# Performance work log

Measured on AMD Instinct MI355X. Metric: run time of the kernel, lower is better.

Reference implementation:

```python
import jax, jax.numpy as jnp
import numpy as np

TEMPERATURE = 0.1
POS_WEIGHT = 0.3
EPS = 1e-8  # torch F.cosine_similarity eps


def setup_inputs() -> dict:
    key = jax.random.key(0)
    k1, k2, k3 = jax.random.split(key, 3)
    B, P, N, D = 256, 4, 1024, 512
    anchor = jax.random.normal(k1, (B, D), dtype=jnp.float32)
    positives = jax.random.normal(k2, (B, P, D), dtype=jnp.float32)
    negatives = jax.random.normal(k3, (B, N, D), dtype=jnp.float32)
    return {"anchor": anchor, "positives": positives, "negatives": negatives}


def _cosine_sim(a, b):
    # a: (B, 1, D), b: (B, N, D) -> (B, N)
    num = jnp.sum(a * b, axis=-1)
    den = jnp.maximum(jnp.linalg.norm(a, axis=-1) * jnp.linalg.norm(b, axis=-1), EPS)
    return num / den


def reference(anchor, positives, negatives):
    num_pos = positives.shape[1]
    a = anchor[:, None, :]                      # (B, 1, D)
    pos_sim = _cosine_sim(a, positives)         # (B, P)
    neg_sim = _cosine_sim(a, negatives)         # (B, N)
    all_sim = jnp.concatenate([pos_sim, neg_sim], axis=1)   # (B, P+N)
    probs = jax.nn.softmax(all_sim / TEMPERATURE, axis=1)   # (B, P+N)

    # rank (0-based) of each column in descending-prob order: argsort-of-argsort
    order = jnp.argsort(-probs, axis=1)         # (B, P+N) indices sorted descending
    ranks = jnp.argsort(order, axis=1)          # rank of each original column

    rr = 1.0 / (ranks[:, :num_pos].astype(jnp.float32) + 1.0)   # (B, P)
    expected_rr = jnp.sum(probs[:, :num_pos] * rr, axis=1)      # (B,)

    loss = -jnp.mean(expected_rr)
    loss = loss + POS_WEIGHT * (1.0 - jnp.mean(pos_sim))
    return loss
```

## Files before the change

kernel.cpp:

```cpp
#include <hip/hip_runtime.h>
#include <math.h>

#define B_DIM 256
#define P_DIM 4
#define N_DIM 1024
#define D_DIM 512
#define NV (P_DIM + N_DIM)
#define INV_TEMP 10.0f
#define POS_W 0.3f
#define EPS_C 1e-8f

__device__ __forceinline__ float wave_sum_f(float v) {
#pragma unroll
  for (int m = 1; m < 64; m <<= 1) v += __shfl_xor(v, m, 64);
  return v;
}

__device__ __forceinline__ float wave_max_f(float v) {
#pragma unroll
  for (int m = 1; m < 64; m <<= 1) v = fmaxf(v, __shfl_xor(v, m, 64));
  return v;
}

__device__ __forceinline__ int wave_sum_i(int v) {
#pragma unroll
  for (int m = 1; m < 64; m <<= 1) v += __shfl_xor(v, m, 64);
  return v;
}

__device__ __forceinline__ float dot4(float4 a, float4 b) {
  return a.x * b.x + a.y * b.y + a.z * b.z + a.w * b.w;
}

__global__ __launch_bounds__(1024) void rr_row_kernel(
    const float* __restrict__ anchor, const float* __restrict__ positives,
    const float* __restrict__ negatives, float* __restrict__ partials) {
  const int b = blockIdx.x;
  const int lane = threadIdx.x & 63;
  const int wave = threadIdx.x >> 6;

  __shared__ float sims[NV];

  const float4* arow = (const float4*)(anchor + (size_t)b * D_DIM);
  const float4 a0 = arow[lane];
  const float4 a1 = arow[lane + 64];
  float asq = dot4(a0, a0) + dot4(a1, a1);
  asq = wave_sum_f(asq);
  const float anorm = sqrtf(asq);

  const float* posrow = positives + (size_t)b * P_DIM * D_DIM;
  const float* negrow = negatives + (size_t)b * N_DIM * D_DIM;

#pragma unroll 1
  for (int it = 0; it < 8; ++it) {
    const int v0 = it * 128 + wave * 8;
    float4 bv[8][2];
#pragma unroll
    for (int i = 0; i < 8; ++i) {
      const int v = v0 + i;
      const float* src = (v < P_DIM) ? (posrow + (size_t)v * D_DIM)
                                     : (negrow + (size_t)(v - P_DIM) * D_DIM);
      const float4* p = (const float4*)src;
      bv[i][0] = p[lane];
      bv[i][1] = p[lane + 64];
    }
    float d[8], bq[8];
#pragma unroll
    for (int i = 0; i < 8; ++i) {
      d[i]  = dot4(a0, bv[i][0]) + dot4(a1, bv[i][1]);
      bq[i] = dot4(bv[i][0], bv[i][0]) + dot4(bv[i][1], bv[i][1]);
    }
#pragma unroll
    for (int i = 0; i < 8; ++i) {
      d[i]  = wave_sum_f(d[i]);
      bq[i] = wave_sum_f(bq[i]);
    }
    if (lane == 0) {
#pragma unroll
      for (int i = 0; i < 8; ++i) {
        const float den = fmaxf(anorm * sqrtf(bq[i]), EPS_C);
        sims[v0 + i] = d[i] / den;
      }
    }
  }

  if (wave == 0) {
#pragma unroll
    for (int i = 0; i < 4; ++i) {
      const int v = 1024 + i;
      const float4* p = (const float4*)(negrow + (size_t)(v - P_DIM) * D_DIM);
      const float4 b0 = p[lane];
      const float4 b1 = p[lane + 64];
      float d  = dot4(a0, b0) + dot4(a1, b1);
      float bq = dot4(b0, b0) + dot4(b1, b1);
      d  = wave_sum_f(d);
      bq = wave_sum_f(bq);
      if (lane == 0) {
        const float den = fmaxf(anorm * sqrtf(bq), EPS_C);
        sims[v] = d / den;
      }
    }
  }
  __syncthreads();

  if (wave == 0) {
    float m = -3.4e38f;
    for (int v = lane; v < NV; v += 64) m = fmaxf(m, sims[v] * INV_TEMP);
    m = wave_max_f(m);
    float Z = 0.0f;
    for (int v = lane; v < NV; v += 64) Z += expf(sims[v] * INV_TEMP - m);
    Z = wave_sum_f(Z);
    const float sp0 = sims[0], sp1 = sims[1], sp2 = sims[2], sp3 = sims[3];
    int c0 = 0, c1 = 0, c2 = 0, c3 = 0;
    for (int v = lane; v < NV; v += 64) {
      const float s = sims[v];
      c0 += (s > sp0);
      c1 += (s > sp1) || (s == sp1 && v < 1);
      c2 += (s > sp2) || (s == sp2 && v < 2);
      c3 += (s > sp3) || (s == sp3 && v < 3);
    }
    c0 = wave_sum_i(c0);
    c1 = wave_sum_i(c1);
    c2 = wave_sum_i(c2);
    c3 = wave_sum_i(c3);
    if (lane == 0) {
      const float invZ = 1.0f / Z;
      const float p0 = expf(sp0 * INV_TEMP - m) * invZ;
      const float p1 = expf(sp1 * INV_TEMP - m) * invZ;
      const float p2 = expf(sp2 * INV_TEMP - m) * invZ;
      const float p3 = expf(sp3 * INV_TEMP - m) * invZ;
      const float err = p0 / (float)(c0 + 1) + p1 / (float)(c1 + 1) +
                        p2 / (float)(c2 + 1) + p3 / (float)(c3 + 1);
      partials[b] = err;
      partials[B_DIM + b] = sp0 + sp1 + sp2 + sp3;
    }
  }
}

__global__ __launch_bounds__(256) void rr_finalize_kernel(
    const float* __restrict__ partials, float* __restrict__ out) {
  const int t = threadIdx.x;
  const int lane = t & 63;
  const int wave = t >> 6;
  float rr = partials[t];
  float ps = partials[B_DIM + t];
  rr = wave_sum_f(rr);
  ps = wave_sum_f(ps);
  __shared__ float srr[4], sps[4];
  if (lane == 0) { srr[wave] = rr; sps[wave] = ps; }
  __syncthreads();
  if (t == 0) {
    const float SRR = srr[0] + srr[1] + srr[2] + srr[3];
    const float SPS = sps[0] + sps[1] + sps[2] + sps[3];
    const float loss =
        -(SRR / (float)B_DIM) +
        POS_W * (1.0f - SPS / (float)(B_DIM * P_DIM));
    out[0] = loss;
  }
}

extern "C" void kernel_launch(void* const* d_in, const int* in_sizes, int n_in,
                              void* d_out, int out_size, void* d_ws, size_t ws_size,
                              hipStream_t stream) {
  const float* anchor = (const float*)d_in[0];
  const float* positives = (const float*)d_in[1];
  const float* negatives = (const float*)d_in[2];
  float* partials = (float*)d_ws;
  float* out = (float*)d_out;

  rr_row_kernel<<<B_DIM, 1024, 0, stream>>>(anchor, positives, negatives, partials);
  rr_finalize_kernel<<<1, 256, 0, stream>>>(partials, out);
}
```

Before: 677.4 us.

## Split similarity computation across many small blocks and add separate rank kernel

The per-row 1024-thread kernel is replaced by a 2D grid of 256-thread blocks, where each wave computes 4 cosine similarities and writes them to a global workspace. A new one-wave-per-row kernel then loads the similarities into registers and computes the softmax and rank counts. The goal is higher occupancy and better latency hiding for the memory-bound 537MB negatives read. The cost is an extra kernel launch, a global round trip for the similarity matrix, and fewer loads in flight per wave.

Result: no change. 677.6 us (+0.0%).

```diff
diff --git a/kernel.cpp b/kernel.cpp
--- a/kernel.cpp
+++ b/kernel.cpp
@@ -9,6 +9,8 @@
 #define INV_TEMP 10.0f
 #define POS_W 0.3f
 #define EPS_C 1e-8f
+#define VPW 4
+#define VBLK 65
 
 __device__ __forceinline__ float wave_sum_f(float v) {
 #pragma unroll
@@ -32,108 +34,112 @@
   return a.x * b.x + a.y * b.y + a.z * b.z + a.w * b.w;
 }
 
-__global__ __launch_bounds__(1024) void rr_row_kernel(
+__global__ __launch_bounds__(256, 8) void sims_kernel(
     const float* __restrict__ anchor, const float* __restrict__ positives,
-    const float* __restrict__ negatives, float* __restrict__ partials) {
-  const int b = blockIdx.x;
+    const float* __restrict__ negatives, float* __restrict__ simsg) {
+  const int b = blockIdx.y;
   const int lane = threadIdx.x & 63;
   const int wave = threadIdx.x >> 6;
-
-  __shared__ float sims[NV];
+  const int v0 = blockIdx.x * (4 * VPW) + wave * VPW;
+  if (v0 >= NV) return;
 
   const float4* arow = (const float4*)(anchor + (size_t)b * D_DIM);
   const float4 a0 = arow[lane];
   const float4 a1 = arow[lane + 64];
+
+  const float* posrow = positives + (size_t)b * P_DIM * D_DIM;
+  const float* negrow = negatives + (size_t)b * N_DIM * D_DIM;
+
   float asq = dot4(a0, a0) + dot4(a1, a1);
   asq = wave_sum_f(asq);
   const float anorm = sqrtf(asq);
 
-  const float* posrow = positives + (size_t)b * P_DIM * D_DIM;
-  const float* negrow = negatives + (size_t)b * N_DIM * D_DIM;
-
-#pragma unroll 1
-  for (int it = 0; it < 8; ++it) {
-    const int v0 = it * 128 + wave * 8;
-    float4 bv[8][2];
+  float out[VPW];
 #pragma unroll
-    for (int i = 0; i < 8; ++i) {
-      const int v = v0 + i;
-      const float* src = (v < P_DIM) ? (posrow + (size_t)v * D_DIM)
-                                     : (negrow + (size_t)(v - P_DIM) * D_DIM);
-      const float4* p = (const float4*)src;
-      bv[i][0] = p[lane];
-      bv[i][1] = p[lane + 64];
-    }
-    float d[8], bq[8];
-#pragma unroll
-    for (int i = 0; i < 8; ++i) {
-      d[i]  = dot4(a0, bv[i][0]) + dot4(a1, bv[i][1]);
-      bq[i] = dot4(bv[i][0], bv[i][0]) + dot4(bv[i][1], bv[i][1]);
-    }
-#pragma unroll
-    for (int i = 0; i < 8; ++i) {
-      d[i]  = wave_sum_f(d[i]);
-      bq[i] = wave_sum_f(bq[i]);
-    }
-    if (lane == 0) {
-#pragma unroll
-      for (int i = 0; i < 8; ++i) {
-        const float den = fmaxf(anorm * sqrtf(bq[i]), EPS_C);
-        sims[v0 + i] = d[i] / den;
-      }
-    }
+  for (int pr = 0; pr < VPW / 2; ++pr) {
+    const int va = v0 + 2 * pr;
+    const int vb = va + 1;
+    const float4* pa = (const float4*)((va < P_DIM)
+                           ? posrow + (size_t)va * D_DIM
+                           : negrow + (size_t)(va - P_DIM) * D_DIM);
+    const float4* pb = (const float4*)((vb < P_DIM)
+                           ? posrow + (size_t)vb * D_DIM
+                           : negrow + (size_t)(vb - P_DIM) * D_DIM);
+    const float4 x0 = pa[lane];
+    const float4 x1 = pa[lane + 64];
+    float da = dot4(a0, x0) + dot4(a1, x1);
+    float qa = dot4(x0, x0) + dot4(x1, x1);
+    const float4 y0 = pb[lane];
+    const float4 y1 = pb[lane + 64];
+    da = wave_sum_f(da);
+    qa = wave_sum_f(qa);
+    float db = dot4(a0, y0) + dot4(a1, y1);
+    float qb = dot4(y0, y0) + dot4(y1, y1);
+    db = wave_sum_f(db);
+    qb = wave_sum_f(qb);
+    out[2 * pr]     = da / fmaxf(anorm * sqrtf(qa), EPS_C);
+    out[2 * pr + 1] = db / fmaxf(anorm * sqrtf(qb), EPS_C);
   }
 
-  if (wave == 0) {
+  if (lane == 0) {
+    *(float4*)(simsg + (size_t)b * NV + v0) =
+        make_float4(out[0], out[1], out[2], out[3]);
+  }
+}
+
+__global__ __launch_bounds__(64) void rank_kernel(
+    const float* __restrict__ simsg, float* __restrict__ partials) {
+  const int b = blockIdx.x;
+  const int lane = threadIdx.x;
+  const float* row = simsg + (size_t)b * NV;
+
+  float s[17];
 #pragma unroll
-    for (int i = 0; i < 4; ++i) {
-      const int v = 1024 + i;
-      const float4* p = (const float4*)(negrow + (size_t)(v - P_DIM) * D_DIM);
-      const float4 b0 = p[lane];
-      const float4 b1 = p[lane + 64];
-      float d  = dot4(a0, b0) + dot4(a1, b1);
-      float bq = dot4(b0, b0) + dot4(b1, b1);
-      d  = wave_sum_f(d);
-      bq = wave_sum_f(bq);
-      if (lane == 0) {
-        const float den = fmaxf(anorm * sqrtf(bq), EPS_C);
-        sims[v] = d / den;
-      }
-    }
+  for (int k = 0; k < 17; ++k) {
+    const int v = lane + 64 * k;
+    s[k] = (v < NV) ? row[v] : -3.4e38f;
   }
-  __syncthreads();
 
-  if (wave == 0) {
-    float m = -3.4e38f;
-    for (int v = lane; v < NV; v += 64) m = fmaxf(m, sims[v] * INV_TEMP);
-    m = wave_max_f(m);
-    float Z = 0.0f;
-    for (int v = lane; v < NV; v += 64) Z += expf(sims[v] * INV_TEMP - m);
-    Z = wave_sum_f(Z);
-    const float sp0 = sims[0], sp1 = sims[1], sp2 = sims[2], sp3 = sims[3];
-    int c0 = 0, c1 = 0, c2 = 0, c3 = 0;
-    for (int v = lane; v < NV; v += 64) {
-      const float s = sims[v];
-      c0 += (s > sp0);
-      c1 += (s > sp1) || (s == sp1 && v < 1);
-      c2 += (s > sp2) || (s == sp2 && v < 2);
-      c3 += (s > sp3) || (s == sp3 && v < 3);
-    }
-    c0 = wave_sum_i(c0);
-    c1 = wave_sum_i(c1);
-    c2 = wave_sum_i(c2);
-    c3 = wave_sum_i(c3);
-    if (lane == 0) {
-      const float invZ = 1.0f / Z;
-      const float p0 = expf(sp0 * INV_TEMP - m) * invZ;
-      const float p1 = expf(sp1 * INV_TEMP - m) * invZ;
-      const float p2 = expf(sp2 * INV_TEMP - m) * invZ;
-      const float p3 = expf(sp3 * INV_TEMP - m) * invZ;
-      const float err = p0 / (float)(c0 + 1) + p1 / (float)(c1 + 1) +
-                        p2 / (float)(c2 + 1) + p3 / (float)(c3 + 1);
-      partials[b] = err;
-      partials[B_DIM + b] = sp0 + sp1 + sp2 + sp3;
-    }
+  float m = -3.4e38f;
+#pragma unroll
+  for (int k = 0; k < 17; ++k) m = fmaxf(m, s[k] * INV_TEMP);
+  m = wave_max_f(m);
+
+  float Z = 0.0f;
+#pragma unroll
+  for (int k = 0; k < 17; ++k) Z += expf(s[k] * INV_TEMP - m);
+  Z = wave_sum_f(Z);
+
+  const float sp0 = __shfl(s[0], 0, 64);
+  const float sp1 = __shfl(s[0], 1, 64);
+  const float sp2 = __shfl(s[0], 2, 64);
+  const float sp3 = __shfl(s[0], 3, 64);
+
+  int c0 = 0, c1 = 0, c2 = 0, c3 = 0;
+#pragma unroll
+  for (int k = 0; k < 17; ++k) {
+    const int v = lane + 64 * k;
+    const float sv = s[k];
+    c0 += (sv > sp0);
+    c1 += (sv > sp1) || (sv == sp1 && v < 1);
+    c2 += (sv > sp2) || (sv == sp2 && v < 2);
+    c3 += (sv > sp3) || (sv == sp3 && v < 3);
+  }
+  c0 = wave_sum_i(c0);
+  c1 = wave_sum_i(c1);
+  c2 = wave_sum_i(c2);
+  c3 = wave_sum_i(c3);
+
+  if (lane == 0) {
+    const float invZ = 1.0f / Z;
+    const float p0 = expf(sp0 * INV_TEMP - m) * invZ;
+    const float p1 = expf(sp1 * INV_TEMP - m) * invZ;
+    const float p2 = expf(sp2 * INV_TEMP - m) * invZ;
+    const float p3 = expf(sp3 * INV_TEMP - m) * invZ;
+    const float err = p0 / (float)(c0 + 1) + p1 / (float)(c1 + 1) +
+                      p2 / (float)(c2 + 1) + p3 / (float)(c3 + 1);
+    partials[b] = err;
+    partials[B_DIM + b] = sp0 + sp1 + sp2 + sp3;
   }
 }
 
@@ -165,9 +171,12 @@
   const float* anchor = (const float*)d_in[0];
   const float* positives = (const float*)d_in[1];
   const float* negatives = (const float*)d_in[2];
-  float* partials = (float*)d_ws;
+  float* simsg = (float*)d_ws;
+  float* partials = (float*)d_ws + (size_t)B_DIM * NV;
   float* out = (float*)d_out;
 
-  rr_row_kernel<<<B_DIM, 1024, 0, stream>>>(anchor, positives, negatives, partials);
+  sims_kernel<<<dim3(VBLK, B_DIM), 256, 0, stream>>>(anchor, positives,
+                                                     negatives, simsg);
+  rank_kernel<<<B_DIM, 64, 0, stream>>>(simsg, partials);
   rr_finalize_kernel<<<1, 256, 0, stream>>>(partials, out);
 }
```
